# Optimization experiments

Measured on AMD Instinct MI355X. Metric: run time of the kernel, lower is better.

The kernel has to match this reference:

```python
import jax, jax.numpy as jnp
import numpy as np

F = 128          # input feature dim
OUT = 128        # out_channel
MAX_DEG = 10
DEG_COUNTS = np.array([25000, 50000, 100000, 150000, 100000, 50000,
                       5000, 5000, 5000, 5000, 5000], dtype=np.int64)  # deg 0..10
OFFSETS = np.concatenate([[0], np.cumsum(DEG_COUNTS)])  # static bucket offsets
N = int(OFFSETS[-1])  # 500000 atoms


def setup_inputs() -> dict:
    key = jax.random.key(0)
    ks = jax.random.split(key, 16)
    inp = {
        "atom_features": jax.random.normal(ks[0], (N, F), dtype=jnp.float32),
        "deg_slice": jnp.stack([jnp.asarray(OFFSETS[:-1]), jnp.asarray(DEG_COUNTS)],
                               axis=1).astype(jnp.int32),
    }
    for d in range(1, MAX_DEG + 1):
        inp[f"adj{d}"] = jax.random.randint(ks[d], (int(DEG_COUNTS[d]), d), 0, N,
                                            dtype=jnp.int32)
    s = 1.0 / np.sqrt(F)
    inp["W0"] = jax.random.normal(ks[11], (F, OUT), dtype=jnp.float32) * s
    inp["b0"] = jnp.zeros((OUT,), dtype=jnp.float32)
    inp["W_rel"] = jax.random.normal(ks[12], (MAX_DEG, F, OUT), dtype=jnp.float32) * s
    inp["b_rel"] = jnp.zeros((MAX_DEG, OUT), dtype=jnp.float32)
    inp["W_self"] = jax.random.normal(ks[13], (MAX_DEG, F, OUT), dtype=jnp.float32) * s
    inp["b_self"] = jnp.zeros((MAX_DEG, OUT), dtype=jnp.float32)
    return inp


def reference(atom_features, deg_slice, adj1, adj2, adj3, adj4, adj5,
              adj6, adj7, adj8, adj9, adj10,
              W0, b0, W_rel, b_rel, W_self, b_self):
    adjs = (adj1, adj2, adj3, adj4, adj5, adj6, adj7, adj8, adj9, adj10)
    outs = [None] * (MAX_DEG + 1)
    # degree-0 atoms: self transform only (uses the last weight in W_list)
    self0 = atom_features[int(OFFSETS[0]):int(OFFSETS[1])]
    outs[0] = self0 @ W0 + b0
    for d in range(1, MAX_DEG + 1):
        # gather neighbor features: [n_d, d, F], mean over the d neighbors
        rel = jnp.mean(atom_features[adjs[d - 1]], axis=1)
        self_a = atom_features[int(OFFSETS[d]):int(OFFSETS[d + 1])]
        outs[d] = (rel @ W_rel[d - 1] + b_rel[d - 1]
                   + self_a @ W_self[d - 1] + b_self[d - 1])
    return jax.nn.relu(jnp.concatenate(outs, axis=0))
```

## Files before the change

### kernel.cpp

```cpp
#include <hip/hip_runtime.h>

typedef float f32x4 __attribute__((ext_vector_type(4)));
typedef __bf16 bf16x8 __attribute__((ext_vector_type(8)));
typedef __bf16 bf16x4 __attribute__((ext_vector_type(4)));

struct AdjPtrs { const int* p[10]; };

__global__ void gc_prep(const float* __restrict__ W0, const float* __restrict__ b0,
                        const float* __restrict__ Wrel, const float* __restrict__ brel,
                        const float* __restrict__ Wself, const float* __restrict__ bself,
                        __bf16* __restrict__ wfrag, float* __restrict__ biasall)
{
    const int id = blockIdx.x * 256 + threadIdx.x;
    {
        const int j    = id & 7;
        const int lane = (id >> 3) & 63;
        const int nt   = (id >> 9) & 7;
        const int ks   = (id >> 12) & 7;
        const int d    = id >> 15;
        const int k = ks * 32 + (lane >> 4) * 8 + j;
        const int n = nt * 16 + (lane & 15);
        float v;
        if (d == 0)      v = (k < 128) ? 0.0f : W0[(k - 128) * 128 + n];
        else if (k < 128) v = Wrel[((d - 1) * 128 + k) * 128 + n];
        else              v = Wself[((d - 1) * 128 + (k - 128)) * 128 + n];
        wfrag[id] = (__bf16)v;
    }
    if (id < 11 * 128) {
        const int dd = id >> 7, c = id & 127;
        biasall[id] = (dd == 0) ? b0[c] : (brel[(dd - 1) * 128 + c] + bself[(dd - 1) * 128 + c]);
    }
}

__device__ __forceinline__ int lds_off(int row, int byteoff) {
    const int chunk = byteoff >> 4;
    return row * 256 + ((chunk ^ (row & 7)) << 4) + (byteoff & 15);
}

template<int D>
__device__ __forceinline__ void stage_rel(const int* __restrict__ adjd,
                                          const float* __restrict__ atom,
                                          char* __restrict__ XsB,
                                          int tile, int cnt, int t)
{
    const int r = t >> 2;
    const int q = t & 3;
    const int lr = tile * 64 + r;

    float buf[32];
    #pragma unroll
    for (int i = 0; i < 32; i++) buf[i] = 0.0f;

    if (lr < cnt) {
        const int* arow = adjd + (size_t)lr * D;
        int idx[D];
        #pragma unroll
        for (int e = 0; e < D; e++) idx[e] = arow[e];
        #pragma unroll
        for (int e = 0; e < D; e++) {
            const f32x4* src = (const f32x4*)(atom + (size_t)idx[e] * 128) + q;
            #pragma unroll
            for (int i = 0; i < 8; i++) {
                const f32x4 v = src[4 * i];
                buf[4*i+0] += v[0]; buf[4*i+1] += v[1];
                buf[4*i+2] += v[2]; buf[4*i+3] += v[3];
            }
        }
        if (D > 1) {
            constexpr float sc = 1.0f / (float)D;
            #pragma unroll
            for (int i = 0; i < 32; i++) buf[i] *= sc;
        }
    }

    #pragma unroll
    for (int i = 0; i < 8; i++) {
        const int g = q + 4 * i;
        bf16x4 pk;
        pk[0] = (__bf16)buf[4*i+0]; pk[1] = (__bf16)buf[4*i+1];
        pk[2] = (__bf16)buf[4*i+2]; pk[3] = (__bf16)buf[4*i+3];
        *(bf16x4*)(XsB + lds_off(r, g * 8)) = pk;
    }
}

__global__ __launch_bounds__(256, 6) void gc_main(
    const float* __restrict__ atom, AdjPtrs adj,
    const __bf16* __restrict__ wfrag, const float* __restrict__ biasall,
    float* __restrict__ out)
{
    __shared__ __bf16 Xs[64 * 128];
    char* XsB = (char*)Xs;

    const int bid = blockIdx.x;
    int d, tb, off, cnt;
    if      (bid < 391)  { d = 0;  tb = 0;    off = 0;      cnt = 25000;  }
    else if (bid < 1173) { d = 1;  tb = 391;  off = 25000;  cnt = 50000;  }
    else if (bid < 2736) { d = 2;  tb = 1173; off = 75000;  cnt = 100000; }
    else if (bid < 5080) { d = 3;  tb = 2736; off = 175000; cnt = 150000; }
    else if (bid < 6643) { d = 4;  tb = 5080; off = 325000; cnt = 100000; }
    else if (bid < 7425) { d = 5;  tb = 6643; off = 425000; cnt = 50000;  }
    else if (bid < 7504) { d = 6;  tb = 7425; off = 475000; cnt = 5000;   }
    else if (bid < 7583) { d = 7;  tb = 7504; off = 480000; cnt = 5000;   }
    else if (bid < 7662) { d = 8;  tb = 7583; off = 485000; cnt = 5000;   }
    else if (bid < 7741) { d = 9;  tb = 7662; off = 490000; cnt = 5000;   }
    else                 { d = 10; tb = 7741; off = 495000; cnt = 5000;   }
    const int tile = bid - tb;
    const int t = threadIdx.x;

    if (d > 0) {
        switch (d) {
            case 1:  stage_rel<1> (adj.p[0], atom, XsB, tile, cnt, t); break;
            case 2:  stage_rel<2> (adj.p[1], atom, XsB, tile, cnt, t); break;
            case 3:  stage_rel<3> (adj.p[2], atom, XsB, tile, cnt, t); break;
            case 4:  stage_rel<4> (adj.p[3], atom, XsB, tile, cnt, t); break;
            case 5:  stage_rel<5> (adj.p[4], atom, XsB, tile, cnt, t); break;
            case 6:  stage_rel<6> (adj.p[5], atom, XsB, tile, cnt, t); break;
            case 7:  stage_rel<7> (adj.p[6], atom, XsB, tile, cnt, t); break;
            case 8:  stage_rel<8> (adj.p[7], atom, XsB, tile, cnt, t); break;
            case 9:  stage_rel<9> (adj.p[8], atom, XsB, tile, cnt, t); break;
            case 10: stage_rel<10>(adj.p[9], atom, XsB, tile, cnt, t); break;
        }
        __syncthreads();
    }

    const int lane = t & 63, wave = t >> 6;
    const int m16  = lane & 15, quad = lane >> 4;
    const int mbase = (wave & 1) * 32;
    const int ntb   = (wave >> 1) * 4;

    f32x4 acc[2][4];
    {
        f32x4 z; z[0] = 0.0f; z[1] = 0.0f; z[2] = 0.0f; z[3] = 0.0f;
        #pragma unroll
        for (int mi = 0; mi < 2; mi++)
            #pragma unroll
            for (int ni = 0; ni < 4; ni++) acc[mi][ni] = z;
    }

    const bf16x8* wbase = (const bf16x8*)wfrag + (size_t)d * 64 * 64 + lane;

    const int lr0 = tile * 64 + mbase + m16;
    const int lr1 = lr0 + 16;
    const float* srow0 = atom + (size_t)(off + (lr0 < cnt ? lr0 : cnt - 1)) * 128;
    const float* srow1 = atom + (size_t)(off + (lr1 < cnt ? lr1 : cnt - 1)) * 128;
    const int kq = quad * 8;

    f32x4 v00 = ((const f32x4*)(srow0 + kq))[0];
    f32x4 v01 = ((const f32x4*)(srow0 + kq))[1];
    f32x4 v10 = ((const f32x4*)(srow1 + kq))[0];
    f32x4 v11 = ((const f32x4*)(srow1 + kq))[1];

    if (d > 0) {
        #pragma unroll
        for (int ks = 0; ks < 4; ks++) {
            const bf16x8 a0 = *(const bf16x8*)(XsB + lds_off(mbase + m16,      ks * 64 + quad * 16));
            const bf16x8 a1 = *(const bf16x8*)(XsB + lds_off(mbase + 16 + m16, ks * 64 + quad * 16));
            #pragma unroll
            for (int ni = 0; ni < 4; ni++) {
                const bf16x8 b = wbase[(size_t)(ks * 8 + ntb + ni) * 64];
                acc[0][ni] = __builtin_amdgcn_mfma_f32_16x16x32_bf16(a0, b, acc[0][ni], 0, 0, 0);
                acc[1][ni] = __builtin_amdgcn_mfma_f32_16x16x32_bf16(a1, b, acc[1][ni], 0, 0, 0);
            }
        }
    }

    #pragma unroll
    for (int ksp = 0; ksp < 4; ksp++) {
        bf16x8 a0, a1;
        #pragma unroll
        for (int j = 0; j < 4; j++) {
            a0[j] = (__bf16)v00[j]; a0[4+j] = (__bf16)v01[j];
            a1[j] = (__bf16)v10[j]; a1[4+j] = (__bf16)v11[j];
        }
        if (ksp < 3) {
            const int k0 = (ksp + 1) * 32 + kq;
            v00 = ((const f32x4*)(srow0 + k0))[0];
            v01 = ((const f32x4*)(srow0 + k0))[1];
            v10 = ((const f32x4*)(srow1 + k0))[0];
            v11 = ((const f32x4*)(srow1 + k0))[1];
        }
        #pragma unroll
        for (int ni = 0; ni < 4; ni++) {
            const bf16x8 b = wbase[(size_t)((ksp + 4) * 8 + ntb + ni) * 64];
            acc[0][ni] = __builtin_amdgcn_mfma_f32_16x16x32_bf16(a0, b, acc[0][ni], 0, 0, 0);
            acc[1][ni] = __builtin_amdgcn_mfma_f32_16x16x32_bf16(a1, b, acc[1][ni], 0, 0, 0);
        }
    }

    #pragma unroll
    for (int ni = 0; ni < 4; ni++) {
        const int col = (ntb + ni) * 16 + m16;
        const float bv = biasall[d * 128 + col];
        #pragma unroll
        for (int mi = 0; mi < 2; mi++) {
            #pragma unroll
            for (int rg = 0; rg < 4; rg++) {
                const int lrow = tile * 64 + mbase + mi * 16 + quad * 4 + rg;
                if (lrow < cnt) {
                    const float v = fmaxf(acc[mi][ni][rg] + bv, 0.0f);
                    __builtin_nontemporal_store(v, out + (size_t)(off + lrow) * 128 + col);
                }
            }
        }
    }
}

extern "C" void kernel_launch(void* const* d_in, const int* in_sizes, int n_in,
                              void* d_out, int out_size, void* d_ws, size_t ws_size,
                              hipStream_t stream) {
    const float* atom = (const float*)d_in[0];
    AdjPtrs adj;
    for (int i = 0; i < 10; i++) adj.p[i] = (const int*)d_in[2 + i];
    const float* W0    = (const float*)d_in[12];
    const float* b0    = (const float*)d_in[13];
    const float* Wrel  = (const float*)d_in[14];
    const float* brel  = (const float*)d_in[15];
    const float* Wself = (const float*)d_in[16];
    const float* bself = (const float*)d_in[17];

    __bf16* wfrag   = (__bf16*)d_ws;
    float*  biasall = (float*)((char*)d_ws + 720896);

    hipLaunchKernelGGL(gc_prep, dim3(1408), dim3(256), 0, stream,
                       W0, b0, Wrel, brel, Wself, bself, wfrag, biasall);
    hipLaunchKernelGGL(gc_main, dim3(7820), dim3(256), 0, stream,
                       atom, adj, wfrag, biasall, (float*)d_out);
}
```

Measured before the change: 661.6 us.

## Pre-convert atom features to bf16 and stage output through LDS for vector stores

Adds a pre-pass that converts all atom features to bf16 in workspace, so the gather and self-row reads in the main kernel move half the bytes. Output is now written through an LDS transpose buffer in two passes, giving coalesced 16-byte nontemporal stores instead of scalar stores. The pre-pass adds a full read of the fp32 features plus a bf16 write, and extra barriers, and only runs when the workspace is large enough. Neighbour sums now accumulate bf16-rounded inputs, which slightly changes numerics.

```diff
diff --git a/kernel.cpp b/kernel.cpp
--- a/kernel.cpp
+++ b/kernel.cpp
@@ -3,6 +3,8 @@
 typedef float f32x4 __attribute__((ext_vector_type(4)));
 typedef __bf16 bf16x8 __attribute__((ext_vector_type(8)));
 typedef __bf16 bf16x4 __attribute__((ext_vector_type(4)));
+
+#define N_ATOMS 500000
 
 struct AdjPtrs { const int* p[10]; };
 
@@ -32,14 +34,30 @@
     }
 }
 
+__global__ __launch_bounds__(256) void gc_conv(const float* __restrict__ atom,
+                                               __bf16* __restrict__ atomb)
+{
+    const long total  = (long)N_ATOMS * 16;
+    const long stride = (long)gridDim.x * 256;
+    for (long i = (long)blockIdx.x * 256 + threadIdx.x; i < total; i += stride) {
+        const f32x4 a = ((const f32x4*)atom)[2 * i];
+        const f32x4 b = ((const f32x4*)atom)[2 * i + 1];
+        bf16x8 o;
+        o[0] = (__bf16)a[0]; o[1] = (__bf16)a[1]; o[2] = (__bf16)a[2]; o[3] = (__bf16)a[3];
+        o[4] = (__bf16)b[0]; o[5] = (__bf16)b[1]; o[6] = (__bf16)b[2]; o[7] = (__bf16)b[3];
+        ((bf16x8*)atomb)[i] = o;
+    }
+}
+
 __device__ __forceinline__ int lds_off(int row, int byteoff) {
     const int chunk = byteoff >> 4;
     return row * 256 + ((chunk ^ (row & 7)) << 4) + (byteoff & 15);
 }
 
-template<int D>
+template<int D, bool BT>
 __device__ __forceinline__ void stage_rel(const int* __restrict__ adjd,
                                           const float* __restrict__ atom,
+                                          const __bf16* __restrict__ atomb,
                                           char* __restrict__ XsB,
                                           int tile, int cnt, int t)
 {
@@ -47,49 +65,91 @@
     const int q = t & 3;
     const int lr = tile * 64 + r;
 
-    float buf[32];
-    #pragma unroll
-    for (int i = 0; i < 32; i++) buf[i] = 0.0f;
-
-    if (lr < cnt) {
-        const int* arow = adjd + (size_t)lr * D;
-        int idx[D];
-        #pragma unroll
-        for (int e = 0; e < D; e++) idx[e] = arow[e];
-        #pragma unroll
-        for (int e = 0; e < D; e++) {
-            const f32x4* src = (const f32x4*)(atom + (size_t)idx[e] * 128) + q;
-            #pragma unroll
-            for (int i = 0; i < 8; i++) {
-                const f32x4 v = src[4 * i];
-                buf[4*i+0] += v[0]; buf[4*i+1] += v[1];
-                buf[4*i+2] += v[2]; buf[4*i+3] += v[3];
-            }
-        }
-        if (D > 1) {
-            constexpr float sc = 1.0f / (float)D;
-            #pragma unroll
-            for (int i = 0; i < 32; i++) buf[i] *= sc;
-        }
-    }
-
-    #pragma unroll
-    for (int i = 0; i < 8; i++) {
-        const int g = q + 4 * i;
-        bf16x4 pk;
-        pk[0] = (__bf16)buf[4*i+0]; pk[1] = (__bf16)buf[4*i+1];
-        pk[2] = (__bf16)buf[4*i+2]; pk[3] = (__bf16)buf[4*i+3];
-        *(bf16x4*)(XsB + lds_off(r, g * 8)) = pk;
-    }
-}
-
+    if constexpr (BT) {
+        bf16x8 outv[4];
+        #pragma unroll
+        for (int i = 0; i < 4; i++)
+            #pragma unroll
+            for (int j = 0; j < 8; j++) outv[i][j] = (__bf16)0.0f;
+
+        if (lr < cnt) {
+            const int* arow = adjd + (size_t)lr * D;
+            int idx[D];
+            #pragma unroll
+            for (int e = 0; e < D; e++) idx[e] = arow[e];
+            if constexpr (D == 1) {
+                const bf16x8* src = (const bf16x8*)(atomb + (size_t)idx[0] * 128);
+                #pragma unroll
+                for (int i = 0; i < 4; i++) outv[i] = src[q + 4 * i];
+            } else {
+                float buf[32];
+                #pragma unroll
+                for (int i = 0; i < 32; i++) buf[i] = 0.0f;
+                #pragma unroll
+                for (int e = 0; e < D; e++) {
+                    const bf16x8* src = (const bf16x8*)(atomb + (size_t)idx[e] * 128);
+                    #pragma unroll
+                    for (int i = 0; i < 4; i++) {
+                        const bf16x8 v = src[q + 4 * i];
+                        #pragma unroll
+                        for (int j = 0; j < 8; j++) buf[8 * i + j] += (float)v[j];
+                    }
+                }
+                constexpr float sc = 1.0f / (float)D;
+                #pragma unroll
+                for (int i = 0; i < 4; i++)
+                    #pragma unroll
+                    for (int j = 0; j < 8; j++) outv[i][j] = (__bf16)(buf[8 * i + j] * sc);
+            }
+        }
+        #pragma unroll
+        for (int i = 0; i < 4; i++)
+            *(bf16x8*)(XsB + lds_off(r, (q + 4 * i) * 16)) = outv[i];
+    } else {
+        float buf[32];
+        #pragma unroll
+        for (int i = 0; i < 32; i++) buf[i] = 0.0f;
+        if (lr < cnt) {
+            const int* arow = adjd + (size_t)lr * D;
+            int idx[D];
+            #pragma unroll
+            for (int e = 0; e < D; e++) idx[e] = arow[e];
+            #pragma unroll
+            for (int e = 0; e < D; e++) {
+                const f32x4* src = (const f32x4*)(atom + (size_t)idx[e] * 128) + q;
+                #pragma unroll
+                for (int i = 0; i < 8; i++) {
+                    const f32x4 v = src[4 * i];
+                    buf[4*i+0] += v[0]; buf[4*i+1] += v[1];
+                    buf[4*i+2] += v[2]; buf[4*i+3] += v[3];
+                }
+            }
+            if (D > 1) {
+                constexpr float sc = 1.0f / (float)D;
+                #pragma unroll
+                for (int i = 0; i < 32; i++) buf[i] *= sc;
+            }
+        }
+        #pragma unroll
+        for (int i = 0; i < 8; i++) {
+            const int g = q + 4 * i;
+            bf16x4 pk;
+            pk[0] = (__bf16)buf[4*i+0]; pk[1] = (__bf16)buf[4*i+1];
+            pk[2] = (__bf16)buf[4*i+2]; pk[3] = (__bf16)buf[4*i+3];
+            *(bf16x4*)(XsB + lds_off(r, g * 8)) = pk;
+        }
+    }
+}
+
+template<bool BT>
 __global__ __launch_bounds__(256, 6) void gc_main(
-    const float* __restrict__ atom, AdjPtrs adj,
-    const __bf16* __restrict__ wfrag, const float* __restrict__ biasall,
+    const float* __restrict__ atom, const __bf16* __restrict__ atomb,
+    AdjPtrs adj, const __bf16* __restrict__ wfrag, const float* __restrict__ biasall,
     float* __restrict__ out)
 {
-    __shared__ __bf16 Xs[64 * 128];
-    char* XsB = (char*)Xs;
+    __shared__ __align__(16) char smem[32 * 132 * 4];
+    char*  XsB = smem;
+    float* Xf  = (float*)smem;
 
     const int bid = blockIdx.x;
     int d, tb, off, cnt;
@@ -109,16 +169,16 @@
 
     if (d > 0) {
         switch (d) {
-            case 1:  stage_rel<1> (adj.p[0], atom, XsB, tile, cnt, t); break;
-            case 2:  stage_rel<2> (adj.p[1], atom, XsB, tile, cnt, t); break;
-            case 3:  stage_rel<3> (adj.p[2], atom, XsB, tile, cnt, t); break;
-            case 4:  stage_rel<4> (adj.p[3], atom, XsB, tile, cnt, t); break;
-            case 5:  stage_rel<5> (adj.p[4], atom, XsB, tile, cnt, t); break;
-            case 6:  stage_rel<6> (adj.p[5], atom, XsB, tile, cnt, t); break;
-            case 7:  stage_rel<7> (adj.p[6], atom, XsB, tile, cnt, t); break;
-            case 8:  stage_rel<8> (adj.p[7], atom, XsB, tile, cnt, t); break;
-            case 9:  stage_rel<9> (adj.p[8], atom, XsB, tile, cnt, t); break;
-            case 10: stage_rel<10>(adj.p[9], atom, XsB, tile, cnt, t); break;
+            case 1:  stage_rel<1,  BT>(adj.p[0], atom, atomb, XsB, tile, cnt, t); break;
+            case 2:  stage_rel<2,  BT>(adj.p[1], atom, atomb, XsB, tile, cnt, t); break;
+            case 3:  stage_rel<3,  BT>(adj.p[2], atom, atomb, XsB, tile, cnt, t); break;
+            case 4:  stage_rel<4,  BT>(adj.p[3], atom, atomb, XsB, tile, cnt, t); break;
+            case 5:  stage_rel<5,  BT>(adj.p[4], atom, atomb, XsB, tile, cnt, t); break;
+            case 6:  stage_rel<6,  BT>(adj.p[5], atom, atomb, XsB, tile, cnt, t); break;
+            case 7:  stage_rel<7,  BT>(adj.p[6], atom, atomb, XsB, tile, cnt, t); break;
+            case 8:  stage_rel<8,  BT>(adj.p[7], atom, atomb, XsB, tile, cnt, t); break;
+            case 9:  stage_rel<9,  BT>(adj.p[8], atom, atomb, XsB, tile, cnt, t); break;
+            case 10: stage_rel<10, BT>(adj.p[9], atom, atomb, XsB, tile, cnt, t); break;
         }
         __syncthreads();
     }
@@ -141,14 +201,26 @@
 
     const int lr0 = tile * 64 + mbase + m16;
     const int lr1 = lr0 + 16;
-    const float* srow0 = atom + (size_t)(off + (lr0 < cnt ? lr0 : cnt - 1)) * 128;
-    const float* srow1 = atom + (size_t)(off + (lr1 < cnt ? lr1 : cnt - 1)) * 128;
-    const int kq = quad * 8;
-
-    f32x4 v00 = ((const f32x4*)(srow0 + kq))[0];
-    f32x4 v01 = ((const f32x4*)(srow0 + kq))[1];
-    f32x4 v10 = ((const f32x4*)(srow1 + kq))[0];
-    f32x4 v11 = ((const f32x4*)(srow1 + kq))[1];
+    const int cl0 = lr0 < cnt ? lr0 : cnt - 1;
+    const int cl1 = lr1 < cnt ? lr1 : cnt - 1;
+    const int kq  = quad * 8;
+
+    const __bf16* srow0b = atomb + (size_t)(off + cl0) * 128;
+    const __bf16* srow1b = atomb + (size_t)(off + cl1) * 128;
+    const float*  srow0f = atom  + (size_t)(off + cl0) * 128;
+    const float*  srow1f = atom  + (size_t)(off + cl1) * 128;
+
+    bf16x8 sa0, sa1;
+    f32x4 v00, v01, v10, v11;
+    if constexpr (BT) {
+        sa0 = *(const bf16x8*)(srow0b + kq);
+        sa1 = *(const bf16x8*)(srow1b + kq);
+    } else {
+        v00 = ((const f32x4*)(srow0f + kq))[0];
+        v01 = ((const f32x4*)(srow0f + kq))[1];
+        v10 = ((const f32x4*)(srow1f + kq))[0];
+        v11 = ((const f32x4*)(srow1f + kq))[1];
+    }
 
     if (d > 0) {
         #pragma unroll
@@ -167,17 +239,25 @@
     #pragma unroll
     for (int ksp = 0; ksp < 4; ksp++) {
         bf16x8 a0, a1;
-        #pragma unroll
-        for (int j = 0; j < 4; j++) {
-            a0[j] = (__bf16)v00[j]; a0[4+j] = (__bf16)v01[j];
-            a1[j] = (__bf16)v10[j]; a1[4+j] = (__bf16)v11[j];
-        }
-        if (ksp < 3) {
-            const int k0 = (ksp + 1) * 32 + kq;
-            v00 = ((const f32x4*)(srow0 + k0))[0];
-            v01 = ((const f32x4*)(srow0 + k0))[1];
-            v10 = ((const f32x4*)(srow1 + k0))[0];
-            v11 = ((const f32x4*)(srow1 + k0))[1];
+        if constexpr (BT) {
+            a0 = sa0; a1 = sa1;
+            if (ksp < 3) {
+                sa0 = *(const bf16x8*)(srow0b + (ksp + 1) * 32 + kq);
+                sa1 = *(const bf16x8*)(srow1b + (ksp + 1) * 32 + kq);
+            }
+        } else {
+            #pragma unroll
+            for (int j = 0; j < 4; j++) {
+                a0[j] = (__bf16)v00[j]; a0[4+j] = (__bf16)v01[j];
+                a1[j] = (__bf16)v10[j]; a1[4+j] = (__bf16)v11[j];
+            }
+            if (ksp < 3) {
+                const int k0 = (ksp + 1) * 32 + kq;
+                v00 = ((const f32x4*)(srow0f + k0))[0];
+                v01 = ((const f32x4*)(srow0f + k0))[1];
+                v10 = ((const f32x4*)(srow1f + k0))[0];
+                v11 = ((const f32x4*)(srow1f + k0))[1];
+            }
         }
         #pragma unroll
         for (int ni = 0; ni < 4; ni++) {
@@ -192,14 +272,35 @@
         const int col = (ntb + ni) * 16 + m16;
         const float bv = biasall[d * 128 + col];
         #pragma unroll
-        for (int mi = 0; mi < 2; mi++) {
-            #pragma unroll
-            for (int rg = 0; rg < 4; rg++) {
-                const int lrow = tile * 64 + mbase + mi * 16 + quad * 4 + rg;
-                if (lrow < cnt) {
-                    const float v = fmaxf(acc[mi][ni][rg] + bv, 0.0f);
-                    __builtin_nontemporal_store(v, out + (size_t)(off + lrow) * 128 + col);
-                }
+        for (int mi = 0; mi < 2; mi++)
+            #pragma unroll
+            for (int rg = 0; rg < 4; rg++)
+                acc[mi][ni][rg] = fmaxf(acc[mi][ni][rg] + bv, 0.0f);
+    }
+
+    #pragma unroll
+    for (int pass = 0; pass < 2; pass++) {
+        __syncthreads();
+        if ((wave & 1) == pass) {
+            #pragma unroll
+            for (int ni = 0; ni < 4; ni++) {
+                const int col = (ntb + ni) * 16 + m16;
+                #pragma unroll
+                for (int mi = 0; mi < 2; mi++)
+                    #pragma unroll
+                    for (int rg = 0; rg < 4; rg++)
+                        Xf[(mi * 16 + quad * 4 + rg) * 132 + col] = acc[mi][ni][rg];
+            }
+        }
+        __syncthreads();
+        #pragma unroll
+        for (int i = 0; i < 4; i++) {
+            const int flat = (i * 256 + t) * 4;
+            const int r = flat >> 7, c = flat & 127;
+            const int lrow = tile * 64 + pass * 32 + r;
+            if (lrow < cnt) {
+                const f32x4 v = *(const f32x4*)(Xf + r * 132 + c);
+                __builtin_nontemporal_store(v, (f32x4*)(out + (size_t)(off + lrow) * 128 + c));
             }
         }
     }
@@ -220,9 +321,19 @@
 
     __bf16* wfrag   = (__bf16*)d_ws;
     float*  biasall = (float*)((char*)d_ws + 720896);
+    __bf16* atomb   = (__bf16*)((char*)d_ws + 726528);
+
+    const size_t need = 726528 + (size_t)N_ATOMS * 128 * 2;
 
     hipLaunchKernelGGL(gc_prep, dim3(1408), dim3(256), 0, stream,
                        W0, b0, Wrel, brel, Wself, bself, wfrag, biasall);
-    hipLaunchKernelGGL(gc_main, dim3(7820), dim3(256), 0, stream,
-                       atom, adj, wfrag, biasall, (float*)d_out);
-}
+
+    if (ws_size >= need) {
+        hipLaunchKernelGGL(gc_conv, dim3(2048), dim3(256), 0, stream, atom, atomb);
+        hipLaunchKernelGGL(gc_main<true>, dim3(7820), dim3(256), 0, stream,
+                           atom, atomb, adj, wfrag, biasall, (float*)d_out);
+    } else {
+        hipLaunchKernelGGL(gc_main<false>, dim3(7820), dim3(256), 0, stream,
+                           atom, atomb, adj, wfrag, biasall, (float*)d_out);
+    }
+}
```

Result: faster. 603.9 us (-8.7%).
